# Optimization experiments

Measured on AMD Instinct MI355X. Metric: run time of the kernel, lower is better.

The kernel has to match this reference:

```python
import jax, jax.numpy as jnp
import numpy as np

NUM_NODES = 120000   # entity count
D = 128              # graph_emb_size
T = 10               # time_steps / train_year
B = 64               # batch of input_ids
R = 4                # num_rel
N = 64               # max neighbors per relation (padded)
C = 64               # TCN channel width (output_size)
I = 64               # influence_emb_size
K = 2                # kernel size
L = 8                # TCN levels (num_channels = [64]*8)


def _causal_conv(x, w, b, d):
    # x: [M, Cin, T], w: [Cout, Cin, k] -> causal dilated conv -> [M, Cout, T]
    pad = (w.shape[-1] - 1) * d
    y = jax.lax.conv_general_dilated(x, w, window_strides=(1,), padding=[(pad, 0)],
                                     rhs_dilation=(d,), dimension_numbers=('NCH', 'OIH', 'NCH'))
    return y + b[None, :, None]


def _tcn_last(x, w1_0, b1_0, w2_0, b2_0, down_w, down_b, w1, b1, w2, b2):
    # Bai-style TemporalConvNet; x: [M, D, T] -> last-step state [M, C]
    y = jax.nn.relu(_causal_conv(x, w1_0, b1_0, 1))
    y = jax.nn.relu(_causal_conv(y, w2_0, b2_0, 1))
    h = jax.nn.relu(y + _causal_conv(x, down_w, down_b, 1))  # 1x1 downsample residual (Cin != C)
    for i in range(1, L):
        d = 2 ** i
        y = jax.nn.relu(_causal_conv(h, w1[i - 1], b1[i - 1], d))
        y = jax.nn.relu(_causal_conv(y, w2[i - 1], b2[i - 1], d))
        h = jax.nn.relu(y + h)
    return h[..., -1]


def setup_inputs() -> dict:
    key = jax.random.key(0)
    ks = jax.random.split(key, 16)
    embeddings = jax.random.normal(ks[0], (T, NUM_NODES, D), jnp.float32)
    # entity -> per-year row index; negative = entity absent that year (zero-padded)
    alignment = jax.random.randint(ks[1], (NUM_NODES, T), -NUM_NODES // 5, NUM_NODES).astype(jnp.int32)
    neighbor_idx = jax.random.randint(ks[2], (B, R, N), 0, NUM_NODES).astype(jnp.int32)
    neighbor_mask = jax.random.randint(ks[3], (B, R, N), 0, 2).astype(bool)
    g = lambda k, sh, s: jax.random.normal(k, sh, jnp.float32) * s
    return {
        'embeddings': embeddings,
        'w1_0': g(ks[4], (R, C, D, K), (2.0 / (D * K)) ** 0.5),
        'b1_0': jnp.zeros((R, C), jnp.float32),
        'w2_0': g(ks[5], (R, C, C, K), (2.0 / (C * K)) ** 0.5),
        'b2_0': jnp.zeros((R, C), jnp.float32),
        'down_w': g(ks[6], (R, C, D, 1), (2.0 / D) ** 0.5),
        'down_b': jnp.zeros((R, C), jnp.float32),
        'w1': g(ks[7], (R, L - 1, C, C, K), (2.0 / (C * K)) ** 0.5),
        'b1': jnp.zeros((R, L - 1, C), jnp.float32),
        'w2': g(ks[8], (R, L - 1, C, C, K), (2.0 / (C * K)) ** 0.5),
        'b2': jnp.zeros((R, L - 1, C), jnp.float32),
        'rel_w': g(ks[9], (R, C, I), (2.0 / (C + I)) ** 0.5),
        'alignment': alignment,
        'neighbor_idx': neighbor_idx,
        'neighbor_mask': neighbor_mask,
    }


def reference(embeddings, w1_0, b1_0, w2_0, b2_0, down_w, down_b, w1, b1, w2, b2,
              rel_w, alignment, neighbor_idx, neighbor_mask):
    seq = alignment[neighbor_idx]                                   # [B,R,N,T]
    valid = (seq >= 0) & neighbor_mask[..., None]                   # per-year + existence mask
    idx = jnp.clip(seq, 0)
    # per-year gather: embeddings[t][idx[...,t]] -> [B,R,N,D,T]
    gath = jax.vmap(lambda e, i: e[i], in_axes=(0, -1), out_axes=-1)(embeddings, idx)
    x = gath * valid[:, :, :, None, :].astype(gath.dtype)           # zero-pad absent years
    x = jnp.transpose(x, (1, 0, 2, 3, 4)).reshape(R, B * N, D, T)   # relation-major, neighbors as batch
    last = jax.vmap(_tcn_last)(x, w1_0, b1_0, w2_0, b2_0, down_w, down_b, w1, b1, w2, b2)  # [R,B*N,C]
    infl = jnp.einsum('rmc,rci->rmi', last, rel_w).reshape(R, B, N, I)
    m = jnp.transpose(neighbor_mask, (1, 0, 2)).astype(infl.dtype)  # [R,B,N] drop padded neighbors
    return jnp.einsum('rbni,rbn->bi', infl, m)                      # sum over neighbors and relations
```

## Files before the change

kernel.cpp:

```cpp
#include <hip/hip_runtime.h>
#include <hip/hip_bf16.h>
#include <stdint.h>

constexpr int NUM_NODES = 120000;
constexpr int Tn = 10;
constexpr int Bb = 64, Rr = 4, Nn = 64, Cc = 64, Ii = 64;
constexpr int G = 8;
constexpr int RSTR  = 147456;
constexpr int OFF0  = 0;
constexpr int OFF1  = 16384;
constexpr int OFF2  = 24576;
constexpr int OFFL0 = 32768;

constexpr int OFF_X  = 0;
constexpr int OFF_H0 = 0;
constexpr int OFF_H1 = 6144;
constexpr int OFF_H2 = 10240;
constexpr int OFF_H3 = 12288;
constexpr int OFF_Y  = 20480;
constexpr int ZOFF   = 30720;
constexpr int SMEMB  = 30976;

typedef __attribute__((ext_vector_type(8))) short bf16x8;
typedef __attribute__((ext_vector_type(4))) float f32x4;
typedef __attribute__((ext_vector_type(4))) short s16x4;

__device__ __forceinline__ short f2bf(float f) {
  __hip_bfloat16 h = __float2bfloat16(f);
  return *reinterpret_cast<short*>(&h);
}
__device__ __forceinline__ float bf2f(short s) {
  union { unsigned int u; float f; } x;
  x.u = ((unsigned int)(unsigned short)s) << 16;
  return x.f;
}

extern "C" __global__ void prep_kernel(const float* __restrict__ w1_0,
                                       const float* __restrict__ w2_0,
                                       const float* __restrict__ down_w,
                                       const float* __restrict__ w1s,
                                       const float* __restrict__ w2s,
                                       short* __restrict__ Wf) {
  int i0 = blockIdx.x * blockDim.x + threadIdx.x;
  int stride = gridDim.x * blockDim.x;
  for (int e = i0; e < Rr * RSTR; e += stride) {
    int r = e / RSTR, q = e - r * RSTR;
    float v;
    if (q < 16384) {
      int j = q & 7, lane = (q >> 3) & 63, ks = (q >> 9) & 3, ct = (q >> 11) & 3, tap = (q >> 13) & 1;
      int cout = ct * 16 + (lane & 15), cin = ks * 32 + (lane >> 4) * 8 + j;
      v = w1_0[((r * 64 + cout) * 128 + cin) * 2 + tap];
    } else if (q < 24576) {
      int q2 = q - 16384;
      int j = q2 & 7, lane = (q2 >> 3) & 63, ks = (q2 >> 9) & 3, ct = (q2 >> 11) & 3;
      int cout = ct * 16 + (lane & 15), cin = ks * 32 + (lane >> 4) * 8 + j;
      v = down_w[(r * 64 + cout) * 128 + cin];
    } else if (q < 32768) {
      int q2 = q - 24576;
      int j = q2 & 7, lane = (q2 >> 3) & 63, ks = (q2 >> 9) & 1, ct = (q2 >> 10) & 3, tap = (q2 >> 12) & 1;
      int cout = ct * 16 + (lane & 15), cin = ks * 32 + (lane >> 4) * 8 + j;
      v = w2_0[((r * 64 + cout) * 64 + cin) * 2 + tap];
    } else {
      int q2 = q - 32768;
      int lc = q2 >> 13;
      int l = lc >> 1, jw = lc & 1;
      int q3 = q2 & 8191;
      int j = q3 & 7, lane = (q3 >> 3) & 63, ks = (q3 >> 9) & 1, ct = (q3 >> 10) & 3, tap = (q3 >> 12) & 1;
      int cout = ct * 16 + (lane & 15), cin = ks * 32 + (lane >> 4) * 8 + j;
      const float* src = jw ? w2s : w1s;
      v = src[(((r * 7 + l) * 64 + cout) * 64 + cin) * 2 + tap];
    }
    Wf[e] = f2bf(v);
  }
}

template <int KSN, int NMT, int NTAP, int ROWB>
__device__ __forceinline__ void conv_sp(const char* __restrict__ sm, int srcOff,
                                        const short* __restrict__ wf1,
                                        const short* __restrict__ wf0,
                                        const float* __restrict__ bias,
                                        const int (&T1)[NMT * 2], const int (&T0)[NMT * 2],
                                        int lane, int ct, f32x4 (&acc)[NMT]) {
  const int c16 = (lane >> 4) * 16;
  const int seq = lane & 7;
  const int hi = (lane & 15) >> 3;
  const int sw = seq << 4;
  float bv[4];
#pragma unroll
  for (int g = 0; g < 4; ++g) bv[g] = bias[ct * 16 + (lane >> 4) * 4 + g];
#pragma unroll
  for (int mt = 0; mt < NMT; ++mt) acc[mt] = (f32x4){bv[0], bv[1], bv[2], bv[3]};
  bf16x8 af1[KSN], af0[KSN];
#pragma unroll
  for (int ks = 0; ks < KSN; ++ks)
    af1[ks] = *(const bf16x8*)(wf1 + ((ct * KSN + ks) * 64 + lane) * 8);
  if (NTAP == 2) {
#pragma unroll
    for (int ks = 0; ks < KSN; ++ks)
      af0[ks] = *(const bf16x8*)(wf0 + ((ct * KSN + ks) * 64 + lane) * 8);
  }
#pragma unroll
  for (int mt = 0; mt < NMT; ++mt) {
    int s1 = hi ? T1[2 * mt + 1] : T1[2 * mt];
    const char* p1 = sm + ((s1 < 0) ? ZOFF : srcOff + (s1 * 8 + seq) * ROWB);
#pragma unroll
    for (int ks = 0; ks < KSN; ++ks) {
      bf16x8 b = *(const bf16x8*)(p1 + ((ks * 64 + c16) ^ sw));
      acc[mt] = __builtin_amdgcn_mfma_f32_16x16x32_bf16(af1[ks], b, acc[mt], 0, 0, 0);
    }
    if (NTAP == 2) {
      int s0 = hi ? T0[2 * mt + 1] : T0[2 * mt];
      const char* p0 = sm + ((s0 < 0) ? ZOFF : srcOff + (s0 * 8 + seq) * ROWB);
#pragma unroll
      for (int ks = 0; ks < KSN; ++ks) {
        bf16x8 b = *(const bf16x8*)(p0 + ((ks * 64 + c16) ^ sw));
        acc[mt] = __builtin_amdgcn_mfma_f32_16x16x32_bf16(af0[ks], b, acc[mt], 0, 0, 0);
      }
    }
  }
}

template <int NMT>
__device__ __forceinline__ void store_sp(char* __restrict__ sm, int dstOff, int lane,
                                         int ct, const f32x4 (&v)[NMT]) {
  const int co = ct * 32 + (lane >> 4) * 8;
#pragma unroll
  for (int mt = 0; mt < NMT; ++mt) {
    int oc = 16 * mt + (lane & 15);
    s16x4 p;
#pragma unroll
    for (int g = 0; g < 4; ++g) p[g] = f2bf(v[mt][g]);
    *(s16x4*)(sm + dstOff + oc * 128 + (co ^ ((oc & 7) << 4))) = p;
  }
}

#define RELU_ALL(A, N)                                        \
  _Pragma("unroll") for (int _t = 0; _t < N; ++_t)            \
      _Pragma("unroll") for (int _g = 0; _g < 4; ++_g)        \
          A[_t][_g] = fmaxf(A[_t][_g], 0.f);

template <int NMT>
__device__ __forceinline__ void resid_sp(const char* __restrict__ sm, int prevOff,
                                         const int (&R)[NMT * 2], int lane, int ct,
                                         f32x4 (&a)[NMT]) {
  const int co = ct * 32 + (lane >> 4) * 8;
  const int seq = lane & 7;
  const int hi = (lane & 15) >> 3;
  const int sw = seq << 4;
#pragma unroll
  for (int mt = 0; mt < NMT; ++mt) {
    int rs = hi ? R[2 * mt + 1] : R[2 * mt];
    const char* p = sm + ((rs < 0) ? ZOFF : prevOff + (rs * 8 + seq) * 128);
    s16x4 q = *(const s16x4*)(p + (co ^ sw));
#pragma unroll
    for (int g = 0; g < 4; ++g)
      a[mt][g] = fmaxf(fmaxf(a[mt][g], 0.f) + bf2f(q[g]), 0.f);
  }
}

extern "C" __global__ void __launch_bounds__(256, 4)
tcn_mfma(const float* __restrict__ emb, const int* __restrict__ align_,
         const int* __restrict__ nidx, const int* __restrict__ nmask,
         const float* __restrict__ b1_0, const float* __restrict__ b2_0,
         const float* __restrict__ down_b, const float* __restrict__ b1s,
         const float* __restrict__ b2s, const short* __restrict__ Wf,
         float* __restrict__ P) {
  __shared__ char sm[SMEMB];
  __shared__ int rowid[80];
  __shared__ float mkv[G];
  __shared__ int mapg[G];
  __shared__ int totv;

  const int tid = threadIdx.x;
  const int lane = tid & 63, ct = tid >> 6;
  const int blk = blockIdx.x;
  const int r = blk >> 9;
  const int blkr = blk & 511;
  const int b = blkr >> 3, chunk = blkr & 7;

  if (tid < 64) {
    int n = tid;
    int msk = nmask[(b * Rr + r) * Nn + n];
    unsigned long long bal = __ballot(msk != 0);
    if (tid < G) mapg[tid] = -1;
    if (tid == 0) totv = (int)__popcll(bal);
    int rank = (int)__popcll(bal & ((1ull << n) - 1ull));
    if (msk != 0 && rank >= chunk * G && rank < chunk * G + G)
      mapg[rank - chunk * G] = n;
  }
  if (tid >= 192 && tid < 224) *(uint64_t*)(sm + ZOFF + (tid - 192) * 8) = 0;
  __syncthreads();
  if (chunk * G >= totv) {
    if (tid < 64) P[((r * Bb + b) * 8 + chunk) * 64 + tid] = 0.f;
    return;
  }

  if (tid < 80) {
    int t = tid >> 3, seq = tid & 7;
    int n2 = mapg[seq];
    int s = -1;
    if (n2 >= 0) {
      int ent = nidx[(b * Rr + r) * Nn + n2];
      s = align_[ent * Tn + t];
    }
    rowid[tid] = (n2 >= 0 && s >= 0) ? s : -1;
    if (t == 0) mkv[seq] = (n2 >= 0) ? 1.0f : 0.0f;
  }
  __syncthreads();

#pragma unroll
  for (int it = 0; it < 5; ++it) {
    int idx = tid + it * 256;
    int col = idx >> 4, d8 = idx & 15;
    int row = rowid[col];
    int t = col >> 3;
    bf16x8 p = {0, 0, 0, 0, 0, 0, 0, 0};
    if (row >= 0) {
      const float* src = emb + ((size_t)t * NUM_NODES + row) * 128 + d8 * 8;
      const float4 v0 = *(const float4*)(src);
      const float4 v1 = *(const float4*)(src + 4);
      p[0] = f2bf(v0.x); p[1] = f2bf(v0.y); p[2] = f2bf(v0.z); p[3] = f2bf(v0.w);
      p[4] = f2bf(v1.x); p[5] = f2bf(v1.y); p[6] = f2bf(v1.z); p[7] = f2bf(v1.w);
    }
    *(bf16x8*)(sm + OFF_X + col * 256 + ((d8 * 16) ^ ((col & 7) << 4))) = p;
  }
  __syncthreads();

  const short* wr = Wf + r * RSTR;

  {
    constexpr int T1[10] = {0, 1, 2, 3, 4, 5, 6, 7, 8, 9};
    constexpr int T0[10] = {-1, 0, 1, 2, 3, 4, 5, 6, 7, 8};
    f32x4 a[5];
    conv_sp<4, 5, 2, 256>(sm, OFF_X, wr + OFF0 + 8192, wr + OFF0, b1_0 + r * 64,
                          T1, T0, lane, ct, a);
    RELU_ALL(a, 5)
    store_sp<5>(sm, OFF_Y, lane, ct, a);
  }
  f32x4 accD[3];
  {
    constexpr int TD[6] = {1, 3, 5, 7, 9, 9};
    conv_sp<4, 3, 1, 256>(sm, OFF_X, wr + OFF1, wr + OFF1, down_b + r * 64,
                          TD, TD, lane, ct, accD);
  }
  __syncthreads();
  {
    constexpr int T1[6] = {1, 3, 5, 7, 9, 9};
    constexpr int T0[6] = {0, 2, 4, 6, 8, 8};
    f32x4 a[3];
    conv_sp<2, 3, 2, 128>(sm, OFF_Y, wr + OFF2 + 4096, wr + OFF2, b2_0 + r * 64,
                          T1, T0, lane, ct, a);
#pragma unroll
    for (int mt = 0; mt < 3; ++mt)
#pragma unroll
      for (int g = 0; g < 4; ++g)
        a[mt][g] = fmaxf(fmaxf(a[mt][g], 0.f) + accD[mt][g], 0.f);
    store_sp<3>(sm, OFF_H0, lane, ct, a);
  }
  __syncthreads();
  {
    constexpr int T1[6] = {0, 1, 2, 3, 4, 4};
    constexpr int T0[6] = {-1, 0, 1, 2, 3, 3};
    f32x4 a[3];
    const short* wb = wr + OFFL0;
    conv_sp<2, 3, 2, 128>(sm, OFF_H0, wb + 4096, wb, b1s + (r * 7 + 0) * 64,
                          T1, T0, lane, ct, a);
    RELU_ALL(a, 3)
    store_sp<3>(sm, OFF_Y, lane, ct, a);
  }
  __syncthreads();
  {
    constexpr int T1[4] = {0, 2, 4, 4};
    constexpr int T0[4] = {-1, 1, 3, 3};
    constexpr int R[4] = {0, 2, 4, 4};
    f32x4 a[2];
    const short* wb = wr + OFFL0 + 8192;
    conv_sp<2, 2, 2, 128>(sm, OFF_Y, wb + 4096, wb, b2s + (r * 7 + 0) * 64,
                          T1, T0, lane, ct, a);
    resid_sp<2>(sm, OFF_H0, R, lane, ct, a);
    store_sp<2>(sm, OFF_H1, lane, ct, a);
  }
  __syncthreads();
  {
    constexpr int T1[4] = {0, 1, 2, 2};
    constexpr int T0[4] = {-1, 0, 1, 1};
    f32x4 a[2];
    const short* wb = wr + OFFL0 + 16384;
    conv_sp<2, 2, 2, 128>(sm, OFF_H1, wb + 4096, wb, b1s + (r * 7 + 1) * 64,
                          T1, T0, lane, ct, a);
    RELU_ALL(a, 2)
    store_sp<2>(sm, OFF_Y, lane, ct, a);
  }
  __syncthreads();
  {
    constexpr int T1[2] = {0, 2};
    constexpr int T0[2] = {-1, 1};
    constexpr int R[2] = {0, 2};
    f32x4 a[1];
    const short* wb = wr + OFFL0 + 16384 + 8192;
    conv_sp<2, 1, 2, 128>(sm, OFF_Y, wb + 4096, wb, b2s + (r * 7 + 1) * 64,
                          T1, T0, lane, ct, a);
    resid_sp<1>(sm, OFF_H1, R, lane, ct, a);
    store_sp<1>(sm, OFF_H2, lane, ct, a);
  }
  __syncthreads();
  {
    constexpr int T1[2] = {0, 1};
    constexpr int T0[2] = {-1, 0};
    f32x4 a[1];
    const short* wb = wr + OFFL0 + 32768;
    conv_sp<2, 1, 2, 128>(sm, OFF_H2, wb + 4096, wb, b1s + (r * 7 + 2) * 64,
                          T1, T0, lane, ct, a);
    RELU_ALL(a, 1)
    store_sp<1>(sm, OFF_Y, lane, ct, a);
  }
  __syncthreads();
  {
    constexpr int T1[2] = {1, 1};
    constexpr int T0[2] = {0, 0};
    constexpr int R[2] = {1, 1};
    f32x4 a[1];
    const short* wb = wr + OFFL0 + 32768 + 8192;
    conv_sp<2, 1, 2, 128>(sm, OFF_Y, wb + 4096, wb, b2s + (r * 7 + 2) * 64,
                          T1, T0, lane, ct, a);
    resid_sp<1>(sm, OFF_H2, R, lane, ct, a);
    store_sp<1>(sm, OFF_H3, lane, ct, a);
  }
  __syncthreads();

  f32x4 hfin[1];
  static constexpr int TA[2] = {0, 0};
#pragma unroll 1
  for (int li = 0; li < 4; ++li) {
    const short* base = wr + OFFL0 + (3 + li) * 16384;
    const int prevOff = OFF_H3 + li * 1024;
    {
      f32x4 a[1];
      conv_sp<2, 1, 1, 128>(sm, prevOff, base + 4096, base + 4096,
                            b1s + (r * 7 + 3 + li) * 64, TA, TA, lane, ct, a);
      RELU_ALL(a, 1)
      store_sp<1>(sm, OFF_Y, lane, ct, a);
    }
    __syncthreads();
    {
      f32x4 a[1];
      conv_sp<2, 1, 1, 128>(sm, OFF_Y, base + 8192 + 4096, base + 8192 + 4096,
                            b2s + (r * 7 + 3 + li) * 64, TA, TA, lane, ct, a);
      resid_sp<1>(sm, prevOff, TA, lane, ct, a);
      if (li < 3) store_sp<1>(sm, prevOff + 1024, lane, ct, a);
      hfin[0] = a[0];
    }
    __syncthreads();
  }

  float mk = ((lane & 15) < 8) ? mkv[lane & 7] : 0.f;
  float s0 = hfin[0][0] * mk, s1 = hfin[0][1] * mk, s2 = hfin[0][2] * mk, s3 = hfin[0][3] * mk;
#pragma unroll
  for (int m2 = 1; m2 <= 4; m2 <<= 1) {
    s0 += __shfl_xor(s0, m2);
    s1 += __shfl_xor(s1, m2);
    s2 += __shfl_xor(s2, m2);
    s3 += __shfl_xor(s3, m2);
  }
  if ((lane & 15) == 0) {
    int base = ((r * Bb + b) * 8 + chunk) * 64 + ct * 16 + (lane >> 4) * 4;
    P[base + 0] = s0;
    P[base + 1] = s1;
    P[base + 2] = s2;
    P[base + 3] = s3;
  }
}

extern "C" __global__ void reduce_kernel(const float* __restrict__ P,
                                         const float* __restrict__ rel_w,
                                         float* __restrict__ out) {
  __shared__ float Sl[Rr * Cc];
  int b = blockIdx.x, i = threadIdx.x;
  for (int idx = i; idx < Rr * Cc; idx += 64) {
    int rr = idx >> 6, cc = idx & 63;
    float s = 0.f;
    for (int p = 0; p < 8; ++p) s += P[((rr * Bb + b) * 8 + p) * 64 + cc];
    Sl[idx] = s;
  }
  __syncthreads();
  float acc = 0.f;
  for (int r = 0; r < Rr; ++r)
#pragma unroll
    for (int cc = 0; cc < 64; ++cc)
      acc += Sl[r * Cc + cc] * rel_w[(r * Cc + cc) * Ii + i];
  out[b * Ii + i] = acc;
}

extern "C" void kernel_launch(void* const* d_in, const int* in_sizes, int n_in,
                              void* d_out, int out_size, void* d_ws, size_t ws_size,
                              hipStream_t stream) {
  const float* emb    = (const float*)d_in[0];
  const float* w1_0   = (const float*)d_in[1];
  const float* b1_0   = (const float*)d_in[2];
  const float* w2_0   = (const float*)d_in[3];
  const float* b2_0   = (const float*)d_in[4];
  const float* down_w = (const float*)d_in[5];
  const float* down_b = (const float*)d_in[6];
  const float* w1s    = (const float*)d_in[7];
  const float* b1s    = (const float*)d_in[8];
  const float* w2s    = (const float*)d_in[9];
  const float* b2s    = (const float*)d_in[10];
  const float* rel_w  = (const float*)d_in[11];
  const int* align_   = (const int*)d_in[12];
  const int* nidx     = (const int*)d_in[13];
  const int* nmask    = (const int*)d_in[14];

  float* P  = (float*)d_ws;
  short* Wf = (short*)((char*)d_ws + 524288);

  prep_kernel<<<768, 256, 0, stream>>>(w1_0, w2_0, down_w, w1s, w2s, Wf);
  tcn_mfma<<<2048, 256, 0, stream>>>(emb, align_, nidx, nmask, b1_0, b2_0, down_b,
                                     b1s, b2s, Wf, P);
  reduce_kernel<<<Bb, Cc, 0, stream>>>(P, rel_w, (float*)d_out);
}
```

Before: 56.96 us.

## Read embeddings directly from global memory into MFMA operands, dropping LDS staging

The first conv layer and the 1x1 downsample conv now load embedding rows straight from global memory into bf16 MFMA B-fragments, using per-lane row offsets. This replaces the cooperative gather of X into shared memory and the barrier that followed. The change frees LDS (shared memory shrinks, which may allow more resident blocks) and removes one sync. In exchange, each embedding row is fetched several times, because the T1 and T0 taps and the downsample conv overlap, so it relies on cache hits and uses less coalesced per-lane loads.

```diff
diff --git a/kernel.cpp b/kernel.cpp
--- a/kernel.cpp
+++ b/kernel.cpp
@@ -12,14 +12,13 @@
 constexpr int OFF2  = 24576;
 constexpr int OFFL0 = 32768;
 
-constexpr int OFF_X  = 0;
-constexpr int OFF_H0 = 0;
+constexpr int OFF_Y  = 0;
 constexpr int OFF_H1 = 6144;
-constexpr int OFF_H2 = 10240;
-constexpr int OFF_H3 = 12288;
-constexpr int OFF_Y  = 20480;
-constexpr int ZOFF   = 30720;
-constexpr int SMEMB  = 30976;
+constexpr int OFF_H0 = 10240;
+constexpr int OFF_H2 = 16384;
+constexpr int OFF_H3 = 18432;
+constexpr int ZOFF   = 23552;
+constexpr int SMEMB  = 23808;
 
 typedef __attribute__((ext_vector_type(8))) short bf16x8;
 typedef __attribute__((ext_vector_type(4))) float f32x4;
@@ -74,6 +73,75 @@
   }
 }
 
+template <int NMT, int NTAP>
+__device__ __forceinline__ void conv_gl(const float* __restrict__ emb,
+                                        const unsigned int (&eo)[10],
+                                        const short* __restrict__ wf1,
+                                        const short* __restrict__ wf0,
+                                        const float* __restrict__ bias,
+                                        const int (&T1)[NMT * 2], const int (&T0)[NMT * 2],
+                                        int lane, int ct, f32x4 (&acc)[NMT]) {
+  const int hi = (lane & 15) >> 3;
+  const int cin0 = (lane >> 4) * 8;
+  float bv[4];
+#pragma unroll
+  for (int g = 0; g < 4; ++g) bv[g] = bias[ct * 16 + (lane >> 4) * 4 + g];
+#pragma unroll
+  for (int mt = 0; mt < NMT; ++mt) acc[mt] = (f32x4){bv[0], bv[1], bv[2], bv[3]};
+  bf16x8 af1[4], af0[4];
+#pragma unroll
+  for (int ks = 0; ks < 4; ++ks)
+    af1[ks] = *(const bf16x8*)(wf1 + ((ct * 4 + ks) * 64 + lane) * 8);
+  if (NTAP == 2) {
+#pragma unroll
+    for (int ks = 0; ks < 4; ++ks)
+      af0[ks] = *(const bf16x8*)(wf0 + ((ct * 4 + ks) * 64 + lane) * 8);
+  }
+#pragma unroll
+  for (int mt = 0; mt < NMT; ++mt) {
+    {
+      unsigned int elo = (T1[2 * mt] >= 0) ? eo[(T1[2 * mt] < 0) ? 0 : T1[2 * mt]] : 0xFFFFFFFFu;
+      unsigned int ehi = (T1[2 * mt + 1] >= 0) ? eo[(T1[2 * mt + 1] < 0) ? 0 : T1[2 * mt + 1]] : 0xFFFFFFFFu;
+      unsigned int e = hi ? ehi : elo;
+      bool val = (e != 0xFFFFFFFFu);
+      const float* bp = emb + (size_t)(val ? e : 0u) * 128 + cin0;
+#pragma unroll
+      for (int ks = 0; ks < 4; ++ks) {
+        bf16x8 bfrag = {0, 0, 0, 0, 0, 0, 0, 0};
+        if (val) {
+          f32x4 v0 = *(const f32x4*)(bp + ks * 32);
+          f32x4 v1 = *(const f32x4*)(bp + ks * 32 + 4);
+          bfrag[0] = f2bf(v0[0]); bfrag[1] = f2bf(v0[1]);
+          bfrag[2] = f2bf(v0[2]); bfrag[3] = f2bf(v0[3]);
+          bfrag[4] = f2bf(v1[0]); bfrag[5] = f2bf(v1[1]);
+          bfrag[6] = f2bf(v1[2]); bfrag[7] = f2bf(v1[3]);
+        }
+        acc[mt] = __builtin_amdgcn_mfma_f32_16x16x32_bf16(af1[ks], bfrag, acc[mt], 0, 0, 0);
+      }
+    }
+    if (NTAP == 2) {
+      unsigned int elo = (T0[2 * mt] >= 0) ? eo[(T0[2 * mt] < 0) ? 0 : T0[2 * mt]] : 0xFFFFFFFFu;
+      unsigned int ehi = (T0[2 * mt + 1] >= 0) ? eo[(T0[2 * mt + 1] < 0) ? 0 : T0[2 * mt + 1]] : 0xFFFFFFFFu;
+      unsigned int e = hi ? ehi : elo;
+      bool val = (e != 0xFFFFFFFFu);
+      const float* bp = emb + (size_t)(val ? e : 0u) * 128 + cin0;
+#pragma unroll
+      for (int ks = 0; ks < 4; ++ks) {
+        bf16x8 bfrag = {0, 0, 0, 0, 0, 0, 0, 0};
+        if (val) {
+          f32x4 v0 = *(const f32x4*)(bp + ks * 32);
+          f32x4 v1 = *(const f32x4*)(bp + ks * 32 + 4);
+          bfrag[0] = f2bf(v0[0]); bfrag[1] = f2bf(v0[1]);
+          bfrag[2] = f2bf(v0[2]); bfrag[3] = f2bf(v0[3]);
+          bfrag[4] = f2bf(v1[0]); bfrag[5] = f2bf(v1[1]);
+          bfrag[6] = f2bf(v1[2]); bfrag[7] = f2bf(v1[3]);
+        }
+        acc[mt] = __builtin_amdgcn_mfma_f32_16x16x32_bf16(af0[ks], bfrag, acc[mt], 0, 0, 0);
+      }
+    }
+  }
+}
+
 template <int KSN, int NMT, int NTAP, int ROWB>
 __device__ __forceinline__ void conv_sp(const char* __restrict__ sm, int srcOff,
                                         const short* __restrict__ wf1,
@@ -208,40 +276,32 @@
   }
   __syncthreads();
 
-#pragma unroll
-  for (int it = 0; it < 5; ++it) {
-    int idx = tid + it * 256;
-    int col = idx >> 4, d8 = idx & 15;
-    int row = rowid[col];
-    int t = col >> 3;
-    bf16x8 p = {0, 0, 0, 0, 0, 0, 0, 0};
-    if (row >= 0) {
-      const float* src = emb + ((size_t)t * NUM_NODES + row) * 128 + d8 * 8;
-      const float4 v0 = *(const float4*)(src);
-      const float4 v1 = *(const float4*)(src + 4);
-      p[0] = f2bf(v0.x); p[1] = f2bf(v0.y); p[2] = f2bf(v0.z); p[3] = f2bf(v0.w);
-      p[4] = f2bf(v1.x); p[5] = f2bf(v1.y); p[6] = f2bf(v1.z); p[7] = f2bf(v1.w);
-    }
-    *(bf16x8*)(sm + OFF_X + col * 256 + ((d8 * 16) ^ ((col & 7) << 4))) = p;
-  }
-  __syncthreads();
+  unsigned int eo[10];
+  {
+    const int seq = lane & 7;
+#pragma unroll
+    for (int t = 0; t < 10; ++t) {
+      int rv = rowid[t * 8 + seq];
+      eo[t] = (rv >= 0) ? (unsigned int)(t * NUM_NODES + rv) : 0xFFFFFFFFu;
+    }
+  }
 
   const short* wr = Wf + r * RSTR;
 
   {
-    constexpr int T1[10] = {0, 1, 2, 3, 4, 5, 6, 7, 8, 9};
-    constexpr int T0[10] = {-1, 0, 1, 2, 3, 4, 5, 6, 7, 8};
+    static constexpr int T1[10] = {0, 1, 2, 3, 4, 5, 6, 7, 8, 9};
+    static constexpr int T0[10] = {-1, 0, 1, 2, 3, 4, 5, 6, 7, 8};
     f32x4 a[5];
-    conv_sp<4, 5, 2, 256>(sm, OFF_X, wr + OFF0 + 8192, wr + OFF0, b1_0 + r * 64,
-                          T1, T0, lane, ct, a);
+    conv_gl<5, 2>(emb, eo, wr + OFF0 + 8192, wr + OFF0, b1_0 + r * 64,
+                  T1, T0, lane, ct, a);
     RELU_ALL(a, 5)
     store_sp<5>(sm, OFF_Y, lane, ct, a);
   }
   f32x4 accD[3];
   {
-    constexpr int TD[6] = {1, 3, 5, 7, 9, 9};
-    conv_sp<4, 3, 1, 256>(sm, OFF_X, wr + OFF1, wr + OFF1, down_b + r * 64,
-                          TD, TD, lane, ct, accD);
+    static constexpr int TD[6] = {1, 3, 5, 7, 9, 9};
+    conv_gl<3, 1>(emb, eo, wr + OFF1, wr + OFF1, down_b + r * 64,
+                  TD, TD, lane, ct, accD);
   }
   __syncthreads();
   {
```

Result: slower. 132.6 us (+132.7%).

## Split waves into channel-pair × time-half tiles so each B fragment feeds two MFMAs

Applied to the files above, without the earlier changes.

Work is no longer split as one 16-channel output tile per wave. Each wave now owns two output-channel tiles and half of the time tiles, so every B fragment loaded from LDS is reused across two MFMAs. This cuts LDS read traffic per MFMA and balances the early, wider layers across the waves. The later narrow layers and the final 4-level loop run redundantly on both wave halves, and writes come only from h==0. That duplicates MFMA work in the tail and raises register pressure from holding two accumulators per tile.

```diff
diff --git a/kernel.cpp b/kernel.cpp
--- a/kernel.cpp
+++ b/kernel.cpp
@@ -74,88 +74,125 @@
   }
 }
 
-template <int KSN, int NMT, int NTAP, int ROWB>
-__device__ __forceinline__ void conv_sp(const char* __restrict__ sm, int srcOff,
+template <int KSN, int MT0, int NL, int NTAP, int ROWB, int NA>
+__device__ __forceinline__ void conv_pp(const char* __restrict__ sm, int srcOff,
                                         const short* __restrict__ wf1,
                                         const short* __restrict__ wf0,
                                         const float* __restrict__ bias,
-                                        const int (&T1)[NMT * 2], const int (&T0)[NMT * 2],
-                                        int lane, int ct, f32x4 (&acc)[NMT]) {
+                                        const int (&T1)[NA], const int (&T0)[NA],
+                                        int lane, int cp, f32x4 (&acc)[NL][2]) {
   const int c16 = (lane >> 4) * 16;
   const int seq = lane & 7;
   const int hi = (lane & 15) >> 3;
   const int sw = seq << 4;
-  float bv[4];
-#pragma unroll
-  for (int g = 0; g < 4; ++g) bv[g] = bias[ct * 16 + (lane >> 4) * 4 + g];
-#pragma unroll
-  for (int mt = 0; mt < NMT; ++mt) acc[mt] = (f32x4){bv[0], bv[1], bv[2], bv[3]};
-  bf16x8 af1[KSN], af0[KSN];
-#pragma unroll
-  for (int ks = 0; ks < KSN; ++ks)
-    af1[ks] = *(const bf16x8*)(wf1 + ((ct * KSN + ks) * 64 + lane) * 8);
-  if (NTAP == 2) {
-#pragma unroll
-    for (int ks = 0; ks < KSN; ++ks)
-      af0[ks] = *(const bf16x8*)(wf0 + ((ct * KSN + ks) * 64 + lane) * 8);
-  }
-#pragma unroll
-  for (int mt = 0; mt < NMT; ++mt) {
-    int s1 = hi ? T1[2 * mt + 1] : T1[2 * mt];
-    const char* p1 = sm + ((s1 < 0) ? ZOFF : srcOff + (s1 * 8 + seq) * ROWB);
-#pragma unroll
-    for (int ks = 0; ks < KSN; ++ks) {
+#pragma unroll
+  for (int i = 0; i < 2; ++i) {
+    float b0 = bias[(2 * cp + i) * 16 + (lane >> 4) * 4 + 0];
+    float b1 = bias[(2 * cp + i) * 16 + (lane >> 4) * 4 + 1];
+    float b2 = bias[(2 * cp + i) * 16 + (lane >> 4) * 4 + 2];
+    float b3 = bias[(2 * cp + i) * 16 + (lane >> 4) * 4 + 3];
+#pragma unroll
+    for (int mt = 0; mt < NL; ++mt) acc[mt][i] = (f32x4){b0, b1, b2, b3};
+  }
+#pragma unroll
+  for (int ks = 0; ks < KSN; ++ks) {
+    bf16x8 a1[2], a0[2];
+#pragma unroll
+    for (int i = 0; i < 2; ++i)
+      a1[i] = *(const bf16x8*)(wf1 + (((2 * cp + i) * KSN + ks) * 64 + lane) * 8);
+    if (NTAP == 2) {
+#pragma unroll
+      for (int i = 0; i < 2; ++i)
+        a0[i] = *(const bf16x8*)(wf0 + (((2 * cp + i) * KSN + ks) * 64 + lane) * 8);
+    }
+#pragma unroll
+    for (int mt = 0; mt < NL; ++mt) {
+      int s1 = hi ? T1[2 * (MT0 + mt) + 1] : T1[2 * (MT0 + mt)];
+      const char* p1 = sm + ((s1 < 0) ? ZOFF : srcOff + (s1 * 8 + seq) * ROWB);
       bf16x8 b = *(const bf16x8*)(p1 + ((ks * 64 + c16) ^ sw));
-      acc[mt] = __builtin_amdgcn_mfma_f32_16x16x32_bf16(af1[ks], b, acc[mt], 0, 0, 0);
-    }
-    if (NTAP == 2) {
-      int s0 = hi ? T0[2 * mt + 1] : T0[2 * mt];
-      const char* p0 = sm + ((s0 < 0) ? ZOFF : srcOff + (s0 * 8 + seq) * ROWB);
-#pragma unroll
-      for (int ks = 0; ks < KSN; ++ks) {
-        bf16x8 b = *(const bf16x8*)(p0 + ((ks * 64 + c16) ^ sw));
-        acc[mt] = __builtin_amdgcn_mfma_f32_16x16x32_bf16(af0[ks], b, acc[mt], 0, 0, 0);
+      acc[mt][0] = __builtin_amdgcn_mfma_f32_16x16x32_bf16(a1[0], b, acc[mt][0], 0, 0, 0);
+      acc[mt][1] = __builtin_amdgcn_mfma_f32_16x16x32_bf16(a1[1], b, acc[mt][1], 0, 0, 0);
+      if (NTAP == 2) {
+        int s0 = hi ? T0[2 * (MT0 + mt) + 1] : T0[2 * (MT0 + mt)];
+        const char* p0 = sm + ((s0 < 0) ? ZOFF : srcOff + (s0 * 8 + seq) * ROWB);
+        bf16x8 b0v = *(const bf16x8*)(p0 + ((ks * 64 + c16) ^ sw));
+        acc[mt][0] = __builtin_amdgcn_mfma_f32_16x16x32_bf16(a0[0], b0v, acc[mt][0], 0, 0, 0);
+        acc[mt][1] = __builtin_amdgcn_mfma_f32_16x16x32_bf16(a0[1], b0v, acc[mt][1], 0, 0, 0);
       }
     }
   }
 }
 
-template <int NMT>
-__device__ __forceinline__ void store_sp(char* __restrict__ sm, int dstOff, int lane,
-                                         int ct, const f32x4 (&v)[NMT]) {
-  const int co = ct * 32 + (lane >> 4) * 8;
-#pragma unroll
-  for (int mt = 0; mt < NMT; ++mt) {
-    int oc = 16 * mt + (lane & 15);
-    s16x4 p;
-#pragma unroll
-    for (int g = 0; g < 4; ++g) p[g] = f2bf(v[mt][g]);
-    *(s16x4*)(sm + dstOff + oc * 128 + (co ^ ((oc & 7) << 4))) = p;
-  }
-}
-
-#define RELU_ALL(A, N)                                        \
+template <int MT0, int NL>
+__device__ __forceinline__ void store_pp(char* __restrict__ sm, int dstOff, int lane,
+                                         int cp, const f32x4 (&v)[NL][2]) {
+  const int sw = (lane & 7) << 4;
+#pragma unroll
+  for (int mt = 0; mt < NL; ++mt) {
+    int oc = 16 * (MT0 + mt) + (lane & 15);
+#pragma unroll
+    for (int i = 0; i < 2; ++i) {
+      int co = (2 * cp + i) * 32 + (lane >> 4) * 8;
+      s16x4 p;
+#pragma unroll
+      for (int g = 0; g < 4; ++g) p[g] = f2bf(v[mt][i][g]);
+      *(s16x4*)(sm + dstOff + oc * 128 + (co ^ sw)) = p;
+    }
+  }
+}
+
+#define RELU_PP(A, N)                                         \
   _Pragma("unroll") for (int _t = 0; _t < N; ++_t)            \
-      _Pragma("unroll") for (int _g = 0; _g < 4; ++_g)        \
-          A[_t][_g] = fmaxf(A[_t][_g], 0.f);
-
-template <int NMT>
-__device__ __forceinline__ void resid_sp(const char* __restrict__ sm, int prevOff,
-                                         const int (&R)[NMT * 2], int lane, int ct,
-                                         f32x4 (&a)[NMT]) {
-  const int co = ct * 32 + (lane >> 4) * 8;
+      _Pragma("unroll") for (int _i = 0; _i < 2; ++_i)        \
+          _Pragma("unroll") for (int _g = 0; _g < 4; ++_g)    \
+              A[_t][_i][_g] = fmaxf(A[_t][_i][_g], 0.f);
+
+template <int MT0, int NL, int NA>
+__device__ __forceinline__ void resid_pp(const char* __restrict__ sm, int prevOff,
+                                         const int (&R)[NA], int lane, int cp,
+                                         f32x4 (&a)[NL][2]) {
   const int seq = lane & 7;
   const int hi = (lane & 15) >> 3;
   const int sw = seq << 4;
 #pragma unroll
-  for (int mt = 0; mt < NMT; ++mt) {
-    int rs = hi ? R[2 * mt + 1] : R[2 * mt];
+  for (int mt = 0; mt < NL; ++mt) {
+    int rs = hi ? R[2 * (MT0 + mt) + 1] : R[2 * (MT0 + mt)];
     const char* p = sm + ((rs < 0) ? ZOFF : prevOff + (rs * 8 + seq) * 128);
-    s16x4 q = *(const s16x4*)(p + (co ^ sw));
-#pragma unroll
-    for (int g = 0; g < 4; ++g)
-      a[mt][g] = fmaxf(fmaxf(a[mt][g], 0.f) + bf2f(q[g]), 0.f);
-  }
+#pragma unroll
+    for (int i = 0; i < 2; ++i) {
+      int co = (2 * cp + i) * 32 + (lane >> 4) * 8;
+      s16x4 q = *(const s16x4*)(p + (co ^ sw));
+#pragma unroll
+      for (int g = 0; g < 4; ++g)
+        a[mt][i][g] = fmaxf(fmaxf(a[mt][i][g], 0.f) + bf2f(q[g]), 0.f);
+    }
+  }
+}
+
+template <int KSN, int MT0, int NL, int NTAP, int ROWB, int NA>
+__device__ __forceinline__ void pass_crs(char* __restrict__ sm, int srcOff, int dstOff,
+                                         const short* __restrict__ wf1,
+                                         const short* __restrict__ wf0,
+                                         const float* __restrict__ bias,
+                                         const int (&T1)[NA], const int (&T0)[NA],
+                                         int lane, int cp) {
+  f32x4 a[NL][2];
+  conv_pp<KSN, MT0, NL, NTAP, ROWB>(sm, srcOff, wf1, wf0, bias, T1, T0, lane, cp, a);
+  RELU_PP(a, NL)
+  store_pp<MT0, NL>(sm, dstOff, lane, cp, a);
+}
+
+template <int KSN, int MT0, int NL, int NTAP, int ROWB, int NA>
+__device__ __forceinline__ void pass_crr(char* __restrict__ sm, int srcOff, int prevOff,
+                                         int dstOff, const short* __restrict__ wf1,
+                                         const short* __restrict__ wf0,
+                                         const float* __restrict__ bias,
+                                         const int (&T1)[NA], const int (&T0)[NA],
+                                         const int (&R)[NA], int lane, int cp) {
+  f32x4 a[NL][2];
+  conv_pp<KSN, MT0, NL, NTAP, ROWB>(sm, srcOff, wf1, wf0, bias, T1, T0, lane, cp, a);
+  resid_pp<MT0, NL>(sm, prevOff, R, lane, cp, a);
+  store_pp<MT0, NL>(sm, dstOff, lane, cp, a);
 }
 
 extern "C" __global__ void __launch_bounds__(256, 4)
@@ -172,7 +209,8 @@
   __shared__ int totv;
 
   const int tid = threadIdx.x;
-  const int lane = tid & 63, ct = tid >> 6;
+  const int lane = tid & 63, wave = tid >> 6;
+  const int cp = wave & 1, h = wave >> 1;
   const int blk = blockIdx.x;
   const int r = blk >> 9;
   const int blkr = blk & 511;
@@ -228,146 +266,173 @@
 
   const short* wr = Wf + r * RSTR;
 
-  {
-    constexpr int T1[10] = {0, 1, 2, 3, 4, 5, 6, 7, 8, 9};
-    constexpr int T0[10] = {-1, 0, 1, 2, 3, 4, 5, 6, 7, 8};
-    f32x4 a[5];
-    conv_sp<4, 5, 2, 256>(sm, OFF_X, wr + OFF0 + 8192, wr + OFF0, b1_0 + r * 64,
-                          T1, T0, lane, ct, a);
-    RELU_ALL(a, 5)
-    store_sp<5>(sm, OFF_Y, lane, ct, a);
-  }
-  f32x4 accD[3];
-  {
-    constexpr int TD[6] = {1, 3, 5, 7, 9, 9};
-    conv_sp<4, 3, 1, 256>(sm, OFF_X, wr + OFF1, wr + OFF1, down_b + r * 64,
-                          TD, TD, lane, ct, accD);
-  }
-  __syncthreads();
-  {
-    constexpr int T1[6] = {1, 3, 5, 7, 9, 9};
-    constexpr int T0[6] = {0, 2, 4, 6, 8, 8};
-    f32x4 a[3];
-    conv_sp<2, 3, 2, 128>(sm, OFF_Y, wr + OFF2 + 4096, wr + OFF2, b2_0 + r * 64,
-                          T1, T0, lane, ct, a);
-#pragma unroll
-    for (int mt = 0; mt < 3; ++mt)
+  static constexpr int T1p1[10] = {0, 1, 2, 3, 4, 5, 6, 7, 8, 9};
+  static constexpr int T0p1[10] = {-1, 0, 1, 2, 3, 4, 5, 6, 7, 8};
+  static constexpr int TDp2[6] = {1, 3, 5, 7, 9, 9};
+  static constexpr int T1p3[6] = {1, 3, 5, 7, 9, 9};
+  static constexpr int T0p3[6] = {0, 2, 4, 6, 8, 8};
+  static constexpr int T1L1a[6] = {0, 1, 2, 3, 4, 4};
+  static constexpr int T0L1a[6] = {-1, 0, 1, 2, 3, 3};
+  static constexpr int T1L1b[4] = {0, 2, 4, 4};
+  static constexpr int T0L1b[4] = {-1, 1, 3, 3};
+  static constexpr int RL1b[4] = {0, 2, 4, 4};
+  static constexpr int T1L2a[4] = {0, 1, 2, 2};
+  static constexpr int T0L2a[4] = {-1, 0, 1, 1};
+  static constexpr int T1L2b[2] = {0, 2};
+  static constexpr int T0L2b[2] = {-1, 1};
+  static constexpr int RL2b[2] = {0, 2};
+  static constexpr int T1L3a[2] = {0, 1};
+  static constexpr int T0L3a[2] = {-1, 0};
+  static constexpr int T1L3b[2] = {1, 1};
+  static constexpr int T0L3b[2] = {0, 0};
+  static constexpr int RL3b[2] = {1, 1};
+  static constexpr int TA[2] = {0, 0};
+
+  f32x4 accD[2][2];
+  if (h == 0) {
+    pass_crs<4, 0, 3, 2, 256>(sm, OFF_X, OFF_Y, wr + OFF0 + 8192, wr + OFF0,
+                              b1_0 + r * 64, T1p1, T0p1, lane, cp);
+    f32x4 aD[2][2];
+    conv_pp<4, 0, 2, 1, 256>(sm, OFF_X, wr + OFF1, wr + OFF1, down_b + r * 64,
+                             TDp2, TDp2, lane, cp, aD);
+#pragma unroll
+    for (int mt = 0; mt < 2; ++mt)
+#pragma unroll
+      for (int i = 0; i < 2; ++i) accD[mt][i] = aD[mt][i];
+  } else {
+    pass_crs<4, 3, 2, 2, 256>(sm, OFF_X, OFF_Y, wr + OFF0 + 8192, wr + OFF0,
+                              b1_0 + r * 64, T1p1, T0p1, lane, cp);
+    f32x4 aD[1][2];
+    conv_pp<4, 2, 1, 1, 256>(sm, OFF_X, wr + OFF1, wr + OFF1, down_b + r * 64,
+                             TDp2, TDp2, lane, cp, aD);
+#pragma unroll
+    for (int i = 0; i < 2; ++i) accD[0][i] = aD[0][i];
+  }
+  __syncthreads();
+
+  if (h == 0) {
+    f32x4 a[2][2];
+    conv_pp<2, 0, 2, 2, 128>(sm, OFF_Y, wr + OFF2 + 4096, wr + OFF2, b2_0 + r * 64,
+                             T1p3, T0p3, lane, cp, a);
+#pragma unroll
+    for (int mt = 0; mt < 2; ++mt)
+#pragma unroll
+      for (int i = 0; i < 2; ++i)
+#pragma unroll
+        for (int g = 0; g < 4; ++g)
+          a[mt][i][g] = fmaxf(fmaxf(a[mt][i][g], 0.f) + accD[mt][i][g], 0.f);
+    store_pp<0, 2>(sm, OFF_H0, lane, cp, a);
+  } else {
+    f32x4 a[1][2];
+    conv_pp<2, 2, 1, 2, 128>(sm, OFF_Y, wr + OFF2 + 4096, wr + OFF2, b2_0 + r * 64,
+                             T1p3, T0p3, lane, cp, a);
+#pragma unroll
+    for (int i = 0; i < 2; ++i)
 #pragma unroll
       for (int g = 0; g < 4; ++g)
-        a[mt][g] = fmaxf(fmaxf(a[mt][g], 0.f) + accD[mt][g], 0.f);
-    store_sp<3>(sm, OFF_H0, lane, ct, a);
-  }
-  __syncthreads();
-  {
-    constexpr int T1[6] = {0, 1, 2, 3, 4, 4};
-    constexpr int T0[6] = {-1, 0, 1, 2, 3, 3};
-    f32x4 a[3];
+        a[0][i][g] = fmaxf(fmaxf(a[0][i][g], 0.f) + accD[0][i][g], 0.f);
+    store_pp<2, 1>(sm, OFF_H0, lane, cp, a);
+  }
+  __syncthreads();
+
+  {
     const short* wb = wr + OFFL0;
-    conv_sp<2, 3, 2, 128>(sm, OFF_H0, wb + 4096, wb, b1s + (r * 7 + 0) * 64,
-                          T1, T0, lane, ct, a);
-    RELU_ALL(a, 3)
-    store_sp<3>(sm, OFF_Y, lane, ct, a);
-  }
-  __syncthreads();
-  {
-    constexpr int T1[4] = {0, 2, 4, 4};
-    constexpr int T0[4] = {-1, 1, 3, 3};
-    constexpr int R[4] = {0, 2, 4, 4};
-    f32x4 a[2];
+    if (h == 0)
+      pass_crs<2, 0, 2, 2, 128>(sm, OFF_H0, OFF_Y, wb + 4096, wb,
+                                b1s + (r * 7 + 0) * 64, T1L1a, T0L1a, lane, cp);
+    else
+      pass_crs<2, 2, 1, 2, 128>(sm, OFF_H0, OFF_Y, wb + 4096, wb,
+                                b1s + (r * 7 + 0) * 64, T1L1a, T0L1a, lane, cp);
+  }
+  __syncthreads();
+  {
     const short* wb = wr + OFFL0 + 8192;
-    conv_sp<2, 2, 2, 128>(sm, OFF_Y, wb + 4096, wb, b2s + (r * 7 + 0) * 64,
-                          T1, T0, lane, ct, a);
-    resid_sp<2>(sm, OFF_H0, R, lane, ct, a);
-    store_sp<2>(sm, OFF_H1, lane, ct, a);
-  }
-  __syncthreads();
-  {
-    constexpr int T1[4] = {0, 1, 2, 2};
-    constexpr int T0[4] = {-1, 0, 1, 1};
-    f32x4 a[2];
+    if (h == 0)
+      pass_crr<2, 0, 1, 2, 128>(sm, OFF_Y, OFF_H0, OFF_H1, wb + 4096, wb,
+                                b2s + (r * 7 + 0) * 64, T1L1b, T0L1b, RL1b, lane, cp);
+    else
+      pass_crr<2, 1, 1, 2, 128>(sm, OFF_Y, OFF_H0, OFF_H1, wb + 4096, wb,
+                                b2s + (r * 7 + 0) * 64, T1L1b, T0L1b, RL1b, lane, cp);
+  }
+  __syncthreads();
+
+  {
     const short* wb = wr + OFFL0 + 16384;
-    conv_sp<2, 2, 2, 128>(sm, OFF_H1, wb + 4096, wb, b1s + (r * 7 + 1) * 64,
-                          T1, T0, lane, ct, a);
-    RELU_ALL(a, 2)
-    store_sp<2>(sm, OFF_Y, lane, ct, a);
-  }
-  __syncthreads();
-  {
-    constexpr int T1[2] = {0, 2};
-    constexpr int T0[2] = {-1, 1};
-    constexpr int R[2] = {0, 2};
-    f32x4 a[1];
+    if (h == 0)
+      pass_crs<2, 0, 1, 2, 128>(sm, OFF_H1, OFF_Y, wb + 4096, wb,
+                                b1s + (r * 7 + 1) * 64, T1L2a, T0L2a, lane, cp);
+    else
+      pass_crs<2, 1, 1, 2, 128>(sm, OFF_H1, OFF_Y, wb + 4096, wb,
+                                b1s + (r * 7 + 1) * 64, T1L2a, T0L2a, lane, cp);
+  }
+  __syncthreads();
+  {
     const short* wb = wr + OFFL0 + 16384 + 8192;
-    conv_sp<2, 1, 2, 128>(sm, OFF_Y, wb + 4096, wb, b2s + (r * 7 + 1) * 64,
-                          T1, T0, lane, ct, a);
-    resid_sp<1>(sm, OFF_H1, R, lane, ct, a);
-    store_sp<1>(sm, OFF_H2, lane, ct, a);
-  }
-  __syncthreads();
-  {
-    constexpr int T1[2] = {0, 1};
-    constexpr int T0[2] = {-1, 0};
-    f32x4 a[1];
+    pass_crr<2, 0, 1, 2, 128>(sm, OFF_Y, OFF_H1, OFF_H2, wb + 4096, wb,
+                              b2s + (r * 7 + 1) * 64, T1L2b, T0L2b, RL2b, lane, cp);
+  }
+  __syncthreads();
+
+  {
     const short* wb = wr + OFFL0 + 32768;
-    conv_sp<2, 1, 2, 128>(sm, OFF_H2, wb + 4096, wb, b1s + (r * 7 + 2) * 64,
-                          T1, T0, lane, ct, a);
-    RELU_ALL(a, 1)
-    store_sp<1>(sm, OFF_Y, lane, ct, a);
-  }
-  __syncthreads();
-  {
-    constexpr int T1[2] = {1, 1};
-    constexpr int T0[2] = {0, 0};
-    constexpr int R[2] = {1, 1};
-    f32x4 a[1];
+    pass_crs<2, 0, 1, 2, 128>(sm, OFF_H2, OFF_Y, wb + 4096, wb,
+                              b1s + (r * 7 + 2) * 64, T1L3a, T0L3a, lane, cp);
+  }
+  __syncthreads();
+  {
     const short* wb = wr + OFFL0 + 32768 + 8192;
-    conv_sp<2, 1, 2, 128>(sm, OFF_Y, wb + 4096, wb, b2s + (r * 7 + 2) * 64,
-                          T1, T0, lane, ct, a);
-    resid_sp<1>(sm, OFF_H2, R, lane, ct, a);
-    store_sp<1>(sm, OFF_H3, lane, ct, a);
-  }
-  __syncthreads();
-
-  f32x4 hfin[1];
-  static constexpr int TA[2] = {0, 0};
+    pass_crr<2, 0, 1, 2, 128>(sm, OFF_Y, OFF_H2, OFF_H3, wb + 4096, wb,
+                              b2s + (r * 7 + 2) * 64, T1L3b, T0L3b, RL3b, lane, cp);
+  }
+  __syncthreads();
+
+  f32x4 hfin[2];
 #pragma unroll 1
   for (int li = 0; li < 4; ++li) {
     const short* base = wr + OFFL0 + (3 + li) * 16384;
     const int prevOff = OFF_H3 + li * 1024;
     {
-      f32x4 a[1];
-      conv_sp<2, 1, 1, 128>(sm, prevOff, base + 4096, base + 4096,
-                            b1s + (r * 7 + 3 + li) * 64, TA, TA, lane, ct, a);
-      RELU_ALL(a, 1)
-      store_sp<1>(sm, OFF_Y, lane, ct, a);
+      f32x4 a[1][2];
+      conv_pp<2, 0, 1, 1, 128>(sm, prevOff, base + 4096, base + 4096,
+                               b1s + (r * 7 + 3 + li) * 64, TA, TA, lane, cp, a);
+      RELU_PP(a, 1)
+      store_pp<0, 1>(sm, OFF_Y, lane, cp, a);
     }
     __syncthreads();
     {
-      f32x4 a[1];
-      conv_sp<2, 1, 1, 128>(sm, OFF_Y, base + 8192 + 4096, base + 8192 + 4096,
-                            b2s + (r * 7 + 3 + li) * 64, TA, TA, lane, ct, a);
-      resid_sp<1>(sm, prevOff, TA, lane, ct, a);
-      if (li < 3) store_sp<1>(sm, prevOff + 1024, lane, ct, a);
-      hfin[0] = a[0];
+      f32x4 a[1][2];
+      conv_pp<2, 0, 1, 1, 128>(sm, OFF_Y, base + 8192 + 4096, base + 8192 + 4096,
+                               b2s + (r * 7 + 3 + li) * 64, TA, TA, lane, cp, a);
+      resid_pp<0, 1>(sm, prevOff, TA, lane, cp, a);
+      if (li < 3) store_pp<0, 1>(sm, prevOff + 1024, lane, cp, a);
+      hfin[0] = a[0][0];
+      hfin[1] = a[0][1];
     }
     __syncthreads();
   }
 
-  float mk = ((lane & 15) < 8) ? mkv[lane & 7] : 0.f;
-  float s0 = hfin[0][0] * mk, s1 = hfin[0][1] * mk, s2 = hfin[0][2] * mk, s3 = hfin[0][3] * mk;
-#pragma unroll
-  for (int m2 = 1; m2 <= 4; m2 <<= 1) {
-    s0 += __shfl_xor(s0, m2);
-    s1 += __shfl_xor(s1, m2);
-    s2 += __shfl_xor(s2, m2);
-    s3 += __shfl_xor(s3, m2);
-  }
-  if ((lane & 15) == 0) {
-    int base = ((r * Bb + b) * 8 + chunk) * 64 + ct * 16 + (lane >> 4) * 4;
-    P[base + 0] = s0;
-    P[base + 1] = s1;
-    P[base + 2] = s2;
-    P[base + 3] = s3;
+  if (h == 0) {
+    float mk = ((lane & 15) < 8) ? mkv[lane & 7] : 0.f;
+#pragma unroll
+    for (int i = 0; i < 2; ++i) {
+      float s0 = hfin[i][0] * mk, s1 = hfin[i][1] * mk;
+      float s2 = hfin[i][2] * mk, s3 = hfin[i][3] * mk;
+#pragma unroll
+      for (int m2 = 1; m2 <= 4; m2 <<= 1) {
+        s0 += __shfl_xor(s0, m2);
+        s1 += __shfl_xor(s1, m2);
+        s2 += __shfl_xor(s2, m2);
+        s3 += __shfl_xor(s3, m2);
+      }
+      if ((lane & 15) == 0) {
+        int ct = 2 * cp + i;
+        int base = ((r * Bb + b) * 8 + chunk) * 64 + ct * 16 + (lane >> 4) * 4;
+        P[base + 0] = s0;
+        P[base + 1] = s1;
+        P[base + 2] = s2;
+        P[base + 3] = s3;
+      }
+    }
   }
 }
 
```

Result: slower. 65.31 us (+14.6%).
